# Kernel optimization log

Measured on AMD Instinct MI355X. Metric: run time of the kernel, lower is better.

Reference implementation:

```python
import jax, jax.numpy as jnp
import numpy as np

N_GRID = 64          # 64x64 grid of patches
N = N_GRID * N_GRID  # 4096 instances
L = 512
L2 = 1024
D = 128
NT = 10              # n_templates
EMB = 48 * 6 * 6     # 1728


def _conv(x, w, b):
    # x: (N,C,H,W), w: (O,I,kh,kw), VALID, stride 1
    y = jax.lax.conv_general_dilated(x, w, (1, 1), 'VALID',
                                     dimension_numbers=('NCHW', 'OIHW', 'NCHW'))
    return y + b[None, :, None, None]


def _maxpool2(x):
    return jax.lax.reduce_window(x, -jnp.inf, jax.lax.max,
                                 (1, 1, 2, 2), (1, 1, 2, 2), 'VALID')


def setup_inputs() -> dict:
    key = jax.random.key(0)
    ks = jax.random.split(key, 16)
    s = 0.05
    rr, cc = jnp.meshgrid(jnp.arange(N_GRID), jnp.arange(N_GRID), indexing='ij')
    positions = jnp.stack([rr.ravel(), cc.ravel()], axis=1).astype(jnp.int32)  # (N,2)
    return {
        'x': jax.random.normal(ks[0], (1, N, 3, 32, 32), jnp.float32),
        'positions': positions,
        'conv1_w': jax.random.normal(ks[1], (36, 3, 4, 4), jnp.float32) * s,
        'conv1_b': jnp.zeros((36,), jnp.float32),
        'conv2_w': jax.random.normal(ks[2], (48, 36, 3, 3), jnp.float32) * s,
        'conv2_b': jnp.zeros((48,), jnp.float32),
        'fc1_w': jax.random.normal(ks[3], (L, EMB), jnp.float32) * s,
        'fc1_b': jnp.zeros((L,), jnp.float32),
        'fc2_w': jax.random.normal(ks[4], (L, L), jnp.float32) * s,
        'fc2_b': jnp.zeros((L,), jnp.float32),
        'nbr_w': jax.random.normal(ks[5], (L, L), jnp.float32) * s,
        'nbr_b': jnp.zeros((L,), jnp.float32),
        'templates': jax.random.normal(ks[6], (NT, L2), jnp.float32),
        'proto_w': jax.random.normal(ks[7], (L2, L2), jnp.float32) * s,
        'proto_b': jnp.zeros((L2,), jnp.float32),
        'ga1_w': jax.random.normal(ks[8], (D, L2), jnp.float32) * s,
        'ga1_b': jnp.zeros((D,), jnp.float32),
        'ga2_w': jax.random.normal(ks[9], (1, D), jnp.float32) * s,
        'ga2_b': jnp.zeros((1,), jnp.float32),
        'cls_w': jax.random.normal(ks[10], (1, L2), jnp.float32) * s,
        'cls_b': jnp.zeros((1,), jnp.float32),
    }


def reference(x, positions, conv1_w, conv1_b, conv2_w, conv2_b,
              fc1_w, fc1_b, fc2_w, fc2_b, nbr_w, nbr_b, templates,
              proto_w, proto_b, ga1_w, ga1_b, ga2_w, ga2_b, cls_w, cls_b):
    temperature = 1.0
    xb = x[0]  # squeeze(0): (N,3,32,32)
    # feature_extractor_part1
    h = _maxpool2(jax.nn.relu(_conv(xb, conv1_w, conv1_b)))   # (N,36,14,14)
    h = _maxpool2(jax.nn.relu(_conv(h, conv2_w, conv2_b)))    # (N,48,6,6)
    h = h.reshape(-1, EMB)
    # feature_extractor_part2 (dropout = identity in eval)
    H = jax.nn.relu(h @ fc1_w.T + fc1_b)
    H = jax.nn.relu(H @ fc2_w.T + fc2_b)                       # (N,L)
    # neighbourhood attention (vectorized padded/masked form of the per-instance loop)
    p = positions.astype(jnp.int32)
    d0 = jnp.abs(p[:, 0][:, None] - p[:, 0][None, :])
    d1 = jnp.abs(p[:, 1][:, None] - p[:, 1][None, :])
    cheb = jnp.maximum(d0, d1)
    mask = (cheb > 0) & (cheb <= 1)                            # (N,N) bool, 8-neighborhood
    has_nbr = mask.any(axis=1)
    n = mask.shape[0]
    mask = jnp.where(has_nbr[:, None], mask, jnp.eye(n, dtype=bool))  # self fallback
    T = jnp.tanh(H @ nbr_w.T + nbr_b)                          # (N,L)
    S = H @ T.T                                                # S[i,j] = h_i . tanh(W h_j + b)
    logits = jnp.where(mask, S, jnp.finfo(S.dtype).min)
    alphas = jax.nn.softmax(logits, axis=1)                    # (N,N)
    nbhd = alphas @ H                                          # (N,L)
    H2 = jnp.concatenate([H, nbhd], axis=1)                    # (N,L2)
    # prototype attention
    P = jnp.tanh(H2 @ proto_w.T + proto_b)                     # (N,L2)
    betas = jax.nn.softmax((P @ templates.T).T / temperature, axis=1)  # (NT,N)
    embs = betas @ H2                                          # (NT,L2)
    # global attention
    g = jnp.tanh(embs @ ga1_w.T + ga1_b) @ ga2_w.T + ga2_b     # (NT,1)
    gammas = jax.nn.softmax(g.T / temperature, axis=1)         # (1,NT)
    M = gammas @ embs                                          # (1,L2)
    A = gammas @ betas                                         # (1,N)
    Y_prob = jax.nn.sigmoid(M @ cls_w.T + cls_b)               # (1,1)
    Y_hat = (Y_prob >= 0.5).astype(jnp.float32)
    return (Y_prob, Y_hat, A)
```

## Files before the change

### kernel.cpp

```cpp
#include <hip/hip_runtime.h>
#include <math.h>

#define NINST 4096

typedef _Float16 half8 __attribute__((ext_vector_type(8)));
typedef _Float16 half4 __attribute__((ext_vector_type(4)));
typedef float floatx4 __attribute__((ext_vector_type(4)));

__global__ void xform_w12(const float* __restrict__ w1, const float* __restrict__ w2,
                          _Float16* __restrict__ w1t, _Float16* __restrict__ w2t) {
  for (int i = blockIdx.x * 256 + threadIdx.x; i < 48 * 64; i += gridDim.x * 256) {
    const int oc = i >> 6, k = i & 63;
    const int ky = k >> 4, r = k & 15, kx = r >> 2, ic = r & 3;
    float v = 0.f;
    if (oc < 36 && ic < 3) v = w1[((oc * 3 + ic) * 4 + ky) * 4 + kx];
    w1t[i] = (_Float16)v;
  }
  for (int i = blockIdx.x * 256 + threadIdx.x; i < 3 * 48 * 128; i += gridDim.x * 256) {
    const int ky = i / 6144, r = i % 6144;
    const int oc = r >> 7, k = r & 127;
    float v = 0.f;
    if (k < 120) {
      const int kx = k / 40, ic = k % 40;
      if (ic < 36) v = w2[((oc * 36 + ic) * 3 + ky) * 3 + kx];
    }
    w2t[i] = (_Float16)v;
  }
}

__launch_bounds__(256, 4)
__global__ void conv_fused(const float* __restrict__ x,
                           const _Float16* __restrict__ w1t_g,
                           const _Float16* __restrict__ w2t_g,
                           const float* __restrict__ b1, const float* __restrict__ b2,
                           _Float16* __restrict__ emb) {
  __shared__ __align__(16) _Float16 x_s[4096];
  __shared__ __align__(16) _Float16 h1_s[7856];
  __shared__ __align__(16) _Float16 h2_s[1728];

  const int n = blockIdx.x, tid = threadIdx.x;
  const int lane = tid & 63, wave = tid >> 6;
  const int quad = lane >> 4, l15 = lane & 15;

  {
    const float* xb = x + (size_t)n * 3072 + tid * 4;
    floatx4 xr0 = __builtin_nontemporal_load((const floatx4*)(xb));
    floatx4 xr1 = __builtin_nontemporal_load((const floatx4*)(xb + 1024));
    floatx4 xr2 = __builtin_nontemporal_load((const floatx4*)(xb + 2048));
    half8 pk0, pk1;
    pk0[0] = (_Float16)xr0[0]; pk0[1] = (_Float16)xr1[0]; pk0[2] = (_Float16)xr2[0]; pk0[3] = (_Float16)0.f;
    pk0[4] = (_Float16)xr0[1]; pk0[5] = (_Float16)xr1[1]; pk0[6] = (_Float16)xr2[1]; pk0[7] = (_Float16)0.f;
    pk1[0] = (_Float16)xr0[2]; pk1[1] = (_Float16)xr1[2]; pk1[2] = (_Float16)xr2[2]; pk1[3] = (_Float16)0.f;
    pk1[4] = (_Float16)xr0[3]; pk1[5] = (_Float16)xr1[3]; pk1[6] = (_Float16)xr2[3]; pk1[7] = (_Float16)0.f;
    *(half8*)&x_s[tid * 16] = pk0;
    *(half8*)&x_s[tid * 16 + 8] = pk1;
    if (tid < 16) h1_s[7840 + tid] = (_Float16)0.f;
  }
  __syncthreads();

  {
    half8 bc[2][3];
#pragma unroll
    for (int c = 0; c < 2; c++)
#pragma unroll
      for (int nt = 0; nt < 3; nt++)
        bc[c][nt] = *(const half8*)&w1t_g[(nt * 16 + l15) * 64 + c * 32 + quad * 8];
    float bia[3];
#pragma unroll
    for (int nt = 0; nt < 3; nt++) {
      const int oc = nt * 16 + l15;
      bia[nt] = (oc < 36) ? b1[oc] : 0.f;
    }
    for (int mt = wave; mt < 49; mt += 4) {
      const int mA = mt * 16 + l15;
      const int ppA = mA >> 2, dA = mA & 3;
      const int yA = 2 * (ppA / 14) + (dA >> 1);
      const int xA = 2 * (ppA % 14) + (dA & 1);
      floatx4 a1[3];
#pragma unroll
      for (int nt = 0; nt < 3; nt++)
#pragma unroll
        for (int r = 0; r < 4; r++) a1[nt][r] = 0.f;
#pragma unroll
      for (int c = 0; c < 2; c++) {
        const int row = yA + c * 2 + (quad >> 1);
        const half8 af = *(const half8*)&x_s[row * 128 + xA * 4 + (quad & 1) * 8];
#pragma unroll
        for (int nt = 0; nt < 3; nt++)
          a1[nt] = __builtin_amdgcn_mfma_f32_16x16x32_f16(af, bc[c][nt], a1[nt], 0, 0, 0);
      }
      const int ppC = mt * 4 + quad;
#pragma unroll
      for (int nt = 0; nt < 3; nt++) {
        const int oc = nt * 16 + l15;
        float v = fmaxf(fmaxf(a1[nt][0], a1[nt][1]), fmaxf(a1[nt][2], a1[nt][3])) + bia[nt];
        v = fmaxf(v, 0.f);
        if (oc < 40) h1_s[ppC * 40 + oc] = (_Float16)v;
      }
    }
  }
  __syncthreads();

  floatx4 acc2[3][3];
#pragma unroll
  for (int a = 0; a < 3; a++)
#pragma unroll
    for (int j = 0; j < 3; j++)
#pragma unroll
      for (int r = 0; r < 4; r++) acc2[a][j][r] = 0.f;

  for (int ky = 0; ky < 3; ky++) {
    half8 bc2[4][3];
#pragma unroll
    for (int c = 0; c < 4; c++)
#pragma unroll
      for (int nt = 0; nt < 3; nt++)
        bc2[c][nt] = *(const half8*)&w2t_g[ky * 6144 + (nt * 16 + l15) * 128 + c * 32 + quad * 8];
#pragma unroll
    for (int mi = 0; mi < 3; mi++) {
      const int mt = wave + 4 * mi;
      if (mt < 9) {
        const int mA = mt * 16 + l15;
        const int ppA = mA >> 2, dA = mA & 3;
        const int y2 = 2 * (ppA / 6) + (dA >> 1);
        const int x2 = 2 * (ppA % 6) + (dA & 1);
        const int rb = ((y2 + ky) * 14 + x2) * 40;
#pragma unroll
        for (int c = 0; c < 4; c++) {
          const half8 af = *(const half8*)&h1_s[rb + c * 32 + quad * 8];
#pragma unroll
          for (int nt = 0; nt < 3; nt++)
            acc2[mi][nt] = __builtin_amdgcn_mfma_f32_16x16x32_f16(af, bc2[c][nt], acc2[mi][nt], 0, 0, 0);
        }
      }
    }
  }

  {
    float bia2[3];
#pragma unroll
    for (int nt = 0; nt < 3; nt++) bia2[nt] = b2[nt * 16 + l15];
#pragma unroll
    for (int mi = 0; mi < 3; mi++) {
      const int mt = wave + 4 * mi;
      if (mt < 9) {
        const int ppC = mt * 4 + quad;
#pragma unroll
        for (int nt = 0; nt < 3; nt++) {
          const int oc = nt * 16 + l15;
          float v = fmaxf(fmaxf(acc2[mi][nt][0], acc2[mi][nt][1]),
                          fmaxf(acc2[mi][nt][2], acc2[mi][nt][3])) + bia2[nt];
          v = fmaxf(v, 0.f);
          h2_s[oc * 36 + ppC] = (_Float16)v;
        }
      }
    }
  }
  __syncthreads();
  if (tid < 216) {
    half8* dst = (half8*)(emb + (size_t)n * 1728);
    dst[tid] = ((const half8*)h2_s)[tid];
  }
}

template <int ACT>
__launch_bounds__(256, 2)
__global__ void gemm_h(const _Float16* __restrict__ A, const float* __restrict__ Bf,
                       const float* __restrict__ bias, _Float16* __restrict__ C,
                       int K, int lda, int ldb, int ldc) {
  __shared__ __align__(16) _Float16 As[2][128 * 72];
  __shared__ __align__(16) _Float16 Bs[2][64 * 72];
  const int tid = threadIdx.x;
  const int m0 = blockIdx.y * 128, n0 = blockIdx.x * 64;
  const int lane = tid & 63, wave = tid >> 6;
  const int quad = lane >> 4, l15 = lane & 15;
  const int wm = (wave >> 1) * 64, wn = (wave & 1) * 32;
  const int arow = tid >> 1, acol = (tid & 1) * 32;
  const int brow = tid >> 2, bcol = (tid & 3) * 16;

  const _Float16* Ap = A + (size_t)(m0 + arow) * lda + acol;
  const float* Bp = Bf + (size_t)(n0 + brow) * ldb + bcol;

  half8 av0 = *(const half8*)(Ap);
  half8 av1 = *(const half8*)(Ap + 8);
  half8 av2 = *(const half8*)(Ap + 16);
  half8 av3 = *(const half8*)(Ap + 24);
  floatx4 bv0 = *(const floatx4*)(Bp);
  floatx4 bv1 = *(const floatx4*)(Bp + 4);
  floatx4 bv2 = *(const floatx4*)(Bp + 8);
  floatx4 bv3 = *(const floatx4*)(Bp + 12);

  floatx4 acc[4][2];
#pragma unroll
  for (int a = 0; a < 4; a++)
#pragma unroll
    for (int j = 0; j < 2; j++)
#pragma unroll
      for (int r = 0; r < 4; r++) acc[a][j][r] = 0.f;

  int buf = 0;
  for (int k0 = 0; k0 < K; k0 += 64) {
    *(half8*)&As[buf][arow * 72 + acol] = av0;
    *(half8*)&As[buf][arow * 72 + acol + 8] = av1;
    *(half8*)&As[buf][arow * 72 + acol + 16] = av2;
    *(half8*)&As[buf][arow * 72 + acol + 24] = av3;
    {
      half8 bh0, bh1;
      bh0[0] = (_Float16)bv0[0]; bh0[1] = (_Float16)bv0[1];
      bh0[2] = (_Float16)bv0[2]; bh0[3] = (_Float16)bv0[3];
      bh0[4] = (_Float16)bv1[0]; bh0[5] = (_Float16)bv1[1];
      bh0[6] = (_Float16)bv1[2]; bh0[7] = (_Float16)bv1[3];
      bh1[0] = (_Float16)bv2[0]; bh1[1] = (_Float16)bv2[1];
      bh1[2] = (_Float16)bv2[2]; bh1[3] = (_Float16)bv2[3];
      bh1[4] = (_Float16)bv3[0]; bh1[5] = (_Float16)bv3[1];
      bh1[6] = (_Float16)bv3[2]; bh1[7] = (_Float16)bv3[3];
      *(half8*)&Bs[buf][brow * 72 + bcol] = bh0;
      *(half8*)&Bs[buf][brow * 72 + bcol + 8] = bh1;
    }
    __syncthreads();
    if (k0 + 64 < K) {
      av0 = *(const half8*)(Ap + k0 + 64);
      av1 = *(const half8*)(Ap + k0 + 64 + 8);
      av2 = *(const half8*)(Ap + k0 + 64 + 16);
      av3 = *(const half8*)(Ap + k0 + 64 + 24);
      bv0 = *(const floatx4*)(Bp + k0 + 64);
      bv1 = *(const floatx4*)(Bp + k0 + 64 + 4);
      bv2 = *(const floatx4*)(Bp + k0 + 64 + 8);
      bv3 = *(const floatx4*)(Bp + k0 + 64 + 12);
    }
#pragma unroll
    for (int ks = 0; ks < 64; ks += 32) {
      half8 af[4], bf[2];
#pragma unroll
      for (int mt = 0; mt < 4; mt++)
        af[mt] = *(const half8*)&As[buf][(wm + mt * 16 + l15) * 72 + ks + quad * 8];
#pragma unroll
      for (int nt = 0; nt < 2; nt++)
        bf[nt] = *(const half8*)&Bs[buf][(wn + nt * 16 + l15) * 72 + ks + quad * 8];
#pragma unroll
      for (int mt = 0; mt < 4; mt++)
#pragma unroll
        for (int nt = 0; nt < 2; nt++)
          acc[mt][nt] = __builtin_amdgcn_mfma_f32_16x16x32_f16(af[mt], bf[nt], acc[mt][nt], 0, 0, 0);
    }
    buf ^= 1;
  }

#pragma unroll
  for (int nt = 0; nt < 2; nt++) {
    const int col = n0 + wn + nt * 16 + l15;
    const float bcolv = bias[col];
#pragma unroll
    for (int mt = 0; mt < 4; mt++) {
#pragma unroll
      for (int r = 0; r < 4; r++) {
        const int row = m0 + wm + mt * 16 + quad * 4 + r;
        float v = acc[mt][nt][r] + bcolv;
        if (ACT == 1) v = fmaxf(v, 0.f);
        if (ACT == 2) v = tanhf(v);
        C[(size_t)row * ldc + col] = (_Float16)v;
      }
    }
  }
}

__launch_bounds__(256)
__global__ void nbhd_k(_Float16* __restrict__ H2, const _Float16* __restrict__ T) {
  const int wid = (blockIdx.x * 256 + threadIdx.x) >> 6;
  const int lane = threadIdx.x & 63;
  const int r = wid >> 6, c = wid & 63;
  const _Float16* hi = H2 + (size_t)wid * 1024;
  float hreg[8];
#pragma unroll
  for (int u = 0; u < 8; u++) hreg[u] = (float)hi[u * 64 + lane];

  float sv[8];
  int jv[8];
  bool ok[8];
  int q = 0;
#pragma unroll
  for (int dr = -1; dr <= 1; dr++)
#pragma unroll
    for (int dc = -1; dc <= 1; dc++) {
      if (dr == 0 && dc == 0) continue;
      const int rr = r + dr, cc = c + dc;
      const bool v = (rr >= 0) && (rr < 64) && (cc >= 0) && (cc < 64);
      const int j = v ? (rr * 64 + cc) : wid;
      const _Float16* tj = T + (size_t)j * 512;
      float s = 0.f;
#pragma unroll
      for (int u = 0; u < 8; u++) s = fmaf(hreg[u], (float)tj[u * 64 + lane], s);
#pragma unroll
      for (int off = 32; off > 0; off >>= 1) s += __shfl_xor(s, off, 64);
      sv[q] = v ? s : -3.4e38f;
      jv[q] = j;
      ok[q] = v;
      q++;
    }

  float m = sv[0];
#pragma unroll
  for (int a = 1; a < 8; a++) m = fmaxf(m, sv[a]);
  float e[8], den = 0.f;
#pragma unroll
  for (int a = 0; a < 8; a++) {
    e[a] = ok[a] ? expf(sv[a] - m) : 0.f;
    den += e[a];
  }
  const float inv = 1.f / den;

  float outv[8];
#pragma unroll
  for (int u = 0; u < 8; u++) outv[u] = 0.f;
#pragma unroll
  for (int a = 0; a < 8; a++) {
    const float al = e[a] * inv;
    const _Float16* hj = H2 + (size_t)jv[a] * 1024;
#pragma unroll
    for (int u = 0; u < 8; u++) outv[u] = fmaf(al, (float)hj[u * 64 + lane], outv[u]);
  }
  _Float16* dst = H2 + (size_t)wid * 1024 + 512;
#pragma unroll
  for (int u = 0; u < 8; u++) dst[u * 64 + lane] = (_Float16)outv[u];
}

__launch_bounds__(256)
__global__ void templ_scores(const _Float16* __restrict__ P, const float* __restrict__ tmpl,
                             float* __restrict__ tl) {
  const int wid = (blockIdx.x * 256 + threadIdx.x) >> 6;
  const int lane = threadIdx.x & 63;
  const _Float16* p = P + (size_t)wid * 1024;
  float pr[16];
#pragma unroll
  for (int u = 0; u < 16; u++) pr[u] = (float)p[u * 64 + lane];
  for (int t = 0; t < 10; t++) {
    const float* tp = tmpl + t * 1024;
    float s = 0.f;
#pragma unroll
    for (int u = 0; u < 16; u++) s = fmaf(pr[u], tp[u * 64 + lane], s);
#pragma unroll
    for (int off = 32; off > 0; off >>= 1) s += __shfl_xor(s, off, 64);
    if (lane == 0) tl[t * NINST + wid] = s;
  }
}

__launch_bounds__(256)
__global__ void softmax_rows(const float* __restrict__ tl, float* __restrict__ betas,
                             float* __restrict__ embs) {
  const int t = blockIdx.x, tid = threadIdx.x;
  __shared__ float red[256];
  for (int i = tid; i < 1024; i += 256) embs[t * 1024 + i] = 0.f;
  const float* row = tl + t * NINST;
  float m = -3.4e38f;
  for (int i = tid; i < NINST; i += 256) m = fmaxf(m, row[i]);
  red[tid] = m;
  __syncthreads();
  for (int s = 128; s > 0; s >>= 1) {
    if (tid < s) red[tid] = fmaxf(red[tid], red[tid + s]);
    __syncthreads();
  }
  m = red[0];
  __syncthreads();
  float sum = 0.f;
  for (int i = tid; i < NINST; i += 256) sum += expf(row[i] - m);
  red[tid] = sum;
  __syncthreads();
  for (int s = 128; s > 0; s >>= 1) {
    if (tid < s) red[tid] += red[tid + s];
    __syncthreads();
  }
  const float inv = 1.f / red[0];
  for (int i = tid; i < NINST; i += 256) betas[t * NINST + i] = expf(row[i] - m) * inv;
}

__launch_bounds__(256)
__global__ void embs_k(const float* __restrict__ betas, const _Float16* __restrict__ H2,
                       float* __restrict__ embs) {
  const int k = blockIdx.x * 256 + threadIdx.x;
  const int nbase = blockIdx.y * 256;
  float acc[10];
#pragma unroll
  for (int t = 0; t < 10; t++) acc[t] = 0.f;
  for (int n = nbase; n < nbase + 256; n++) {
    const float v = (float)H2[(size_t)n * 1024 + k];
#pragma unroll
    for (int t = 0; t < 10; t++) acc[t] = fmaf(betas[t * NINST + n], v, acc[t]);
  }
#pragma unroll
  for (int t = 0; t < 10; t++) atomicAdd(&embs[t * 1024 + k], acc[t]);
}

__launch_bounds__(256)
__global__ void ga1_k(const float* __restrict__ embs, const float* __restrict__ ga1_w,
                      const float* __restrict__ ga1_b, float* __restrict__ hh) {
  const int d = blockIdx.x, tid = threadIdx.x;
  const int wave = tid >> 6, lane = tid & 63;
  __shared__ float part[4][10];

  float acc[10];
#pragma unroll
  for (int t = 0; t < 10; t++) acc[t] = 0.f;
#pragma unroll
  for (int kk = 0; kk < 4; kk++) {
    const int k = kk * 256 + tid;
    const float wv = ga1_w[(size_t)d * 1024 + k];
#pragma unroll
    for (int t = 0; t < 10; t++) acc[t] = fmaf(wv, embs[t * 1024 + k], acc[t]);
  }
#pragma unroll
  for (int t = 0; t < 10; t++) {
#pragma unroll
    for (int off = 32; off > 0; off >>= 1) acc[t] += __shfl_xor(acc[t], off, 64);
  }
  if (lane == 0) {
#pragma unroll
    for (int t = 0; t < 10; t++) part[wave][t] = acc[t];
  }
  __syncthreads();
  if (tid < 10) {
    const float s = part[0][tid] + part[1][tid] + part[2][tid] + part[3][tid];
    hh[tid * 128 + d] = tanhf(s + ga1_b[d]);
  }
}

__launch_bounds__(256)
__global__ void ga2_k(const float* __restrict__ hh, const float* __restrict__ ga2_w,
                      const float* __restrict__ ga2_b, const float* __restrict__ embs,
                      const float* __restrict__ cls_w, const float* __restrict__ cls_b,
                      float* __restrict__ gam_ws, float* __restrict__ out) {
  __shared__ float g_s[10], gam_s[10];
  __shared__ float red[256];
  const int tid = threadIdx.x;
  const int wave = tid >> 6, lane = tid & 63;

  if (wave == 0) {
    for (int t = 0; t < 10; t++) {
      float s = hh[t * 128 + lane] * ga2_w[lane] + hh[t * 128 + 64 + lane] * ga2_w[64 + lane];
#pragma unroll
      for (int off = 32; off > 0; off >>= 1) s += __shfl_xor(s, off, 64);
      if (lane == 0) g_s[t] = s + ga2_b[0];
    }
  }
  __syncthreads();
  if (tid == 0) {
    float m = g_s[0];
    for (int t = 1; t < 10; t++) m = fmaxf(m, g_s[t]);
    float sum = 0.f;
    for (int t = 0; t < 10; t++) sum += expf(g_s[t] - m);
    for (int t = 0; t < 10; t++) {
      gam_s[t] = expf(g_s[t] - m) / sum;
      gam_ws[t] = gam_s[t];
    }
  }
  __syncthreads();

  float partl = 0.f;
  for (int k = tid; k < 1024; k += 256) {
    float a = 0.f;
#pragma unroll
    for (int t = 0; t < 10; t++) a = fmaf(gam_s[t], embs[t * 1024 + k], a);
    partl = fmaf(a, cls_w[k], partl);
  }
  red[tid] = partl;
  __syncthreads();
  for (int s = 128; s > 0; s >>= 1) {
    if (tid < s) red[tid] += red[tid + s];
    __syncthreads();
  }
  if (tid == 0) {
    const float z = red[0] + cls_b[0];
    const float yp = 1.f / (1.f + expf(-z));
    out[0] = yp;
    out[1] = (yp >= 0.5f) ? 1.f : 0.f;
  }
}

__launch_bounds__(256)
__global__ void a_k(const float* __restrict__ betas, const float* __restrict__ gam,
                    float* __restrict__ outA) {
  const int n = blockIdx.x * 256 + threadIdx.x;
  float a = 0.f;
#pragma unroll
  for (int t = 0; t < 10; t++) a = fmaf(gam[t], betas[t * NINST + n], a);
  outA[n] = a;
}

extern "C" void kernel_launch(void* const* d_in, const int* in_sizes, int n_in,
                              void* d_out, int out_size, void* d_ws, size_t ws_size,
                              hipStream_t stream) {
  const float* x       = (const float*)d_in[0];
  const float* w1      = (const float*)d_in[2];
  const float* b1      = (const float*)d_in[3];
  const float* w2      = (const float*)d_in[4];
  const float* b2      = (const float*)d_in[5];
  const float* fc1_w   = (const float*)d_in[6];
  const float* fc1_b   = (const float*)d_in[7];
  const float* fc2_w   = (const float*)d_in[8];
  const float* fc2_b   = (const float*)d_in[9];
  const float* nbr_w   = (const float*)d_in[10];
  const float* nbr_b   = (const float*)d_in[11];
  const float* tmpl    = (const float*)d_in[12];
  const float* proto_w = (const float*)d_in[13];
  const float* proto_b = (const float*)d_in[14];
  const float* ga1_w   = (const float*)d_in[15];
  const float* ga1_b   = (const float*)d_in[16];
  const float* ga2_w   = (const float*)d_in[17];
  const float* ga2_b   = (const float*)d_in[18];
  const float* cls_w   = (const float*)d_in[19];
  const float* cls_b   = (const float*)d_in[20];
  float* out = (float*)d_out;

  char* w = (char*)d_ws;
  _Float16* embh = (_Float16*)w;  w += (size_t)4096 * 1728 * 2;
  _Float16* H1h  = (_Float16*)w;  w += (size_t)4096 * 512 * 2;
  _Float16* H2h  = (_Float16*)w;  w += (size_t)4096 * 1024 * 2;
  _Float16* TbH  = (_Float16*)w;  w += (size_t)4096 * 512 * 2;
  _Float16* PH   = (_Float16*)w;  w += (size_t)4096 * 1024 * 2;
  _Float16* w1tG = (_Float16*)w;  w += (size_t)48 * 64 * 2;
  _Float16* w2tG = (_Float16*)w;  w += (size_t)3 * 48 * 128 * 2;
  float* tl   = (float*)w;        w += (size_t)10 * NINST * 4;
  float* bet  = (float*)w;        w += (size_t)10 * NINST * 4;
  float* embs = (float*)w;        w += (size_t)10 * 1024 * 4;
  float* hhw  = (float*)w;        w += (size_t)10 * 128 * 4;
  float* gam  = (float*)w;        w += 256;

  xform_w12<<<64, 256, 0, stream>>>(w1, w2, w1tG, w2tG);
  conv_fused<<<NINST, 256, 0, stream>>>(x, w1tG, w2tG, b1, b2, embh);

  gemm_h<1><<<dim3(8, 32), 256, 0, stream>>>(embh, fc1_w, fc1_b, H1h, 1728, 1728, 1728, 512);
  gemm_h<1><<<dim3(8, 32), 256, 0, stream>>>(H1h, fc2_w, fc2_b, H2h, 512, 512, 512, 1024);
  gemm_h<2><<<dim3(8, 32), 256, 0, stream>>>(H2h, nbr_w, nbr_b, TbH, 512, 1024, 512, 512);
  nbhd_k<<<1024, 256, 0, stream>>>(H2h, TbH);
  gemm_h<2><<<dim3(16, 32), 256, 0, stream>>>(H2h, proto_w, proto_b, PH, 1024, 1024, 1024, 1024);
  templ_scores<<<1024, 256, 0, stream>>>(PH, tmpl, tl);
  softmax_rows<<<10, 256, 0, stream>>>(tl, bet, embs);
  embs_k<<<dim3(4, 16), 256, 0, stream>>>(bet, H2h, embs);
  ga1_k<<<128, 256, 0, stream>>>(embs, ga1_w, ga1_b, hhw);
  ga2_k<<<1, 256, 0, stream>>>(hhw, ga2_w, ga2_b, embs, cls_w, cls_b, gam, out);
  a_k<<<16, 256, 0, stream>>>(bet, gam, out + 2);
}
```

Baseline: 369.1 us.

## Fuse template scoring into proto GEMM, shrink GEMM tiles, batch conv instances

After: 381.5 us. +3.4%, slower.

```diff
diff --git a/kernel.cpp b/kernel.cpp
--- a/kernel.cpp
+++ b/kernel.cpp
@@ -8,7 +8,8 @@
 typedef float floatx4 __attribute__((ext_vector_type(4)));
 
 __global__ void xform_w12(const float* __restrict__ w1, const float* __restrict__ w2,
-                          _Float16* __restrict__ w1t, _Float16* __restrict__ w2t) {
+                          _Float16* __restrict__ w1t, _Float16* __restrict__ w2t,
+                          float* __restrict__ tl) {
   for (int i = blockIdx.x * 256 + threadIdx.x; i < 48 * 64; i += gridDim.x * 256) {
     const int oc = i >> 6, k = i & 63;
     const int ky = k >> 4, r = k & 15, kx = r >> 2, ic = r & 3;
@@ -26,35 +27,39 @@
     }
     w2t[i] = (_Float16)v;
   }
-}
-
-__launch_bounds__(256, 4)
+  for (int i = blockIdx.x * 256 + threadIdx.x; i < 10 * NINST; i += gridDim.x * 256)
+    tl[i] = 0.f;
+}
+
+__launch_bounds__(256, 2)
 __global__ void conv_fused(const float* __restrict__ x,
                            const _Float16* __restrict__ w1t_g,
                            const _Float16* __restrict__ w2t_g,
                            const float* __restrict__ b1, const float* __restrict__ b2,
                            _Float16* __restrict__ emb) {
-  __shared__ __align__(16) _Float16 x_s[4096];
-  __shared__ __align__(16) _Float16 h1_s[7856];
-  __shared__ __align__(16) _Float16 h2_s[1728];
-
-  const int n = blockIdx.x, tid = threadIdx.x;
+  __shared__ __align__(16) _Float16 x_s[8192];
+  __shared__ __align__(16) _Float16 h1_s[15712];
+
+  const int n0 = blockIdx.x * 2, tid = threadIdx.x;
   const int lane = tid & 63, wave = tid >> 6;
   const int quad = lane >> 4, l15 = lane & 15;
 
   {
-    const float* xb = x + (size_t)n * 3072 + tid * 4;
-    floatx4 xr0 = __builtin_nontemporal_load((const floatx4*)(xb));
-    floatx4 xr1 = __builtin_nontemporal_load((const floatx4*)(xb + 1024));
-    floatx4 xr2 = __builtin_nontemporal_load((const floatx4*)(xb + 2048));
-    half8 pk0, pk1;
-    pk0[0] = (_Float16)xr0[0]; pk0[1] = (_Float16)xr1[0]; pk0[2] = (_Float16)xr2[0]; pk0[3] = (_Float16)0.f;
-    pk0[4] = (_Float16)xr0[1]; pk0[5] = (_Float16)xr1[1]; pk0[6] = (_Float16)xr2[1]; pk0[7] = (_Float16)0.f;
-    pk1[0] = (_Float16)xr0[2]; pk1[1] = (_Float16)xr1[2]; pk1[2] = (_Float16)xr2[2]; pk1[3] = (_Float16)0.f;
-    pk1[4] = (_Float16)xr0[3]; pk1[5] = (_Float16)xr1[3]; pk1[6] = (_Float16)xr2[3]; pk1[7] = (_Float16)0.f;
-    *(half8*)&x_s[tid * 16] = pk0;
-    *(half8*)&x_s[tid * 16 + 8] = pk1;
-    if (tid < 16) h1_s[7840 + tid] = (_Float16)0.f;
+#pragma unroll
+    for (int inst = 0; inst < 2; inst++) {
+      const float* xb = x + (size_t)(n0 + inst) * 3072 + tid * 4;
+      floatx4 xr0 = __builtin_nontemporal_load((const floatx4*)(xb));
+      floatx4 xr1 = __builtin_nontemporal_load((const floatx4*)(xb + 1024));
+      floatx4 xr2 = __builtin_nontemporal_load((const floatx4*)(xb + 2048));
+      half8 pk0, pk1;
+      pk0[0] = (_Float16)xr0[0]; pk0[1] = (_Float16)xr1[0]; pk0[2] = (_Float16)xr2[0]; pk0[3] = (_Float16)0.f;
+      pk0[4] = (_Float16)xr0[1]; pk0[5] = (_Float16)xr1[1]; pk0[6] = (_Float16)xr2[1]; pk0[7] = (_Float16)0.f;
+      pk1[0] = (_Float16)xr0[2]; pk1[1] = (_Float16)xr1[2]; pk1[2] = (_Float16)xr2[2]; pk1[3] = (_Float16)0.f;
+      pk1[4] = (_Float16)xr0[3]; pk1[5] = (_Float16)xr1[3]; pk1[6] = (_Float16)xr2[3]; pk1[7] = (_Float16)0.f;
+      *(half8*)&x_s[inst * 4096 + tid * 16] = pk0;
+      *(half8*)&x_s[inst * 4096 + tid * 16 + 8] = pk1;
+    }
+    if (tid < 16) { h1_s[7840 + tid] = (_Float16)0.f; h1_s[7856 + 7840 + tid] = (_Float16)0.f; }
   }
   __syncthreads();
 
@@ -71,75 +76,83 @@
       const int oc = nt * 16 + l15;
       bia[nt] = (oc < 36) ? b1[oc] : 0.f;
     }
-    for (int mt = wave; mt < 49; mt += 4) {
-      const int mA = mt * 16 + l15;
-      const int ppA = mA >> 2, dA = mA & 3;
-      const int yA = 2 * (ppA / 14) + (dA >> 1);
-      const int xA = 2 * (ppA % 14) + (dA & 1);
-      floatx4 a1[3];
-#pragma unroll
-      for (int nt = 0; nt < 3; nt++)
-#pragma unroll
-        for (int r = 0; r < 4; r++) a1[nt][r] = 0.f;
-#pragma unroll
-      for (int c = 0; c < 2; c++) {
-        const int row = yA + c * 2 + (quad >> 1);
-        const half8 af = *(const half8*)&x_s[row * 128 + xA * 4 + (quad & 1) * 8];
-#pragma unroll
-        for (int nt = 0; nt < 3; nt++)
-          a1[nt] = __builtin_amdgcn_mfma_f32_16x16x32_f16(af, bc[c][nt], a1[nt], 0, 0, 0);
-      }
-      const int ppC = mt * 4 + quad;
-#pragma unroll
-      for (int nt = 0; nt < 3; nt++) {
-        const int oc = nt * 16 + l15;
-        float v = fmaxf(fmaxf(a1[nt][0], a1[nt][1]), fmaxf(a1[nt][2], a1[nt][3])) + bia[nt];
-        v = fmaxf(v, 0.f);
-        if (oc < 40) h1_s[ppC * 40 + oc] = (_Float16)v;
-      }
-    }
-  }
-  __syncthreads();
-
-  floatx4 acc2[3][3];
-#pragma unroll
-  for (int a = 0; a < 3; a++)
-#pragma unroll
-    for (int j = 0; j < 3; j++)
-#pragma unroll
-      for (int r = 0; r < 4; r++) acc2[a][j][r] = 0.f;
-
-  for (int ky = 0; ky < 3; ky++) {
-    half8 bc2[4][3];
-#pragma unroll
-    for (int c = 0; c < 4; c++)
-#pragma unroll
-      for (int nt = 0; nt < 3; nt++)
-        bc2[c][nt] = *(const half8*)&w2t_g[ky * 6144 + (nt * 16 + l15) * 128 + c * 32 + quad * 8];
-#pragma unroll
-    for (int mi = 0; mi < 3; mi++) {
-      const int mt = wave + 4 * mi;
-      if (mt < 9) {
+#pragma unroll
+    for (int inst = 0; inst < 2; inst++) {
+      const _Float16* xin = x_s + inst * 4096;
+      _Float16* h1o = h1_s + inst * 7856;
+      for (int mt = wave; mt < 49; mt += 4) {
         const int mA = mt * 16 + l15;
         const int ppA = mA >> 2, dA = mA & 3;
-        const int y2 = 2 * (ppA / 6) + (dA >> 1);
-        const int x2 = 2 * (ppA % 6) + (dA & 1);
-        const int rb = ((y2 + ky) * 14 + x2) * 40;
-#pragma unroll
-        for (int c = 0; c < 4; c++) {
-          const half8 af = *(const half8*)&h1_s[rb + c * 32 + quad * 8];
+        const int yA = 2 * (ppA / 14) + (dA >> 1);
+        const int xA = 2 * (ppA % 14) + (dA & 1);
+        floatx4 a1[3];
+#pragma unroll
+        for (int nt = 0; nt < 3; nt++)
+#pragma unroll
+          for (int r = 0; r < 4; r++) a1[nt][r] = 0.f;
+#pragma unroll
+        for (int c = 0; c < 2; c++) {
+          const int row = yA + c * 2 + (quad >> 1);
+          const half8 af = *(const half8*)&xin[row * 128 + xA * 4 + (quad & 1) * 8];
 #pragma unroll
           for (int nt = 0; nt < 3; nt++)
-            acc2[mi][nt] = __builtin_amdgcn_mfma_f32_16x16x32_f16(af, bc2[c][nt], acc2[mi][nt], 0, 0, 0);
+            a1[nt] = __builtin_amdgcn_mfma_f32_16x16x32_f16(af, bc[c][nt], a1[nt], 0, 0, 0);
+        }
+        const int ppC = mt * 4 + quad;
+#pragma unroll
+        for (int nt = 0; nt < 3; nt++) {
+          const int oc = nt * 16 + l15;
+          float v = fmaxf(fmaxf(a1[nt][0], a1[nt][1]), fmaxf(a1[nt][2], a1[nt][3])) + bia[nt];
+          v = fmaxf(v, 0.f);
+          if (oc < 40) h1o[ppC * 40 + oc] = (_Float16)v;
         }
       }
     }
   }
-
-  {
-    float bia2[3];
-#pragma unroll
-    for (int nt = 0; nt < 3; nt++) bia2[nt] = b2[nt * 16 + l15];
+  __syncthreads();
+
+  float bia2[3];
+#pragma unroll
+  for (int nt = 0; nt < 3; nt++) bia2[nt] = b2[nt * 16 + l15];
+
+#pragma unroll
+  for (int inst = 0; inst < 2; inst++) {
+    const _Float16* h1i = h1_s + inst * 7856;
+    _Float16* h2o = x_s + inst * 1728;
+    floatx4 acc2[3][3];
+#pragma unroll
+    for (int a = 0; a < 3; a++)
+#pragma unroll
+      for (int j = 0; j < 3; j++)
+#pragma unroll
+        for (int r = 0; r < 4; r++) acc2[a][j][r] = 0.f;
+
+    for (int ky = 0; ky < 3; ky++) {
+      half8 bc2[4][3];
+#pragma unroll
+      for (int c = 0; c < 4; c++)
+#pragma unroll
+        for (int nt = 0; nt < 3; nt++)
+          bc2[c][nt] = *(const half8*)&w2t_g[ky * 6144 + (nt * 16 + l15) * 128 + c * 32 + quad * 8];
+#pragma unroll
+      for (int mi = 0; mi < 3; mi++) {
+        const int mt = wave + 4 * mi;
+        if (mt < 9) {
+          const int mA = mt * 16 + l15;
+          const int ppA = mA >> 2, dA = mA & 3;
+          const int y2 = 2 * (ppA / 6) + (dA >> 1);
+          const int x2 = 2 * (ppA % 6) + (dA & 1);
+          const int rb = ((y2 + ky) * 14 + x2) * 40;
+#pragma unroll
+          for (int c = 0; c < 4; c++) {
+            const half8 af = *(const half8*)&h1i[rb + c * 32 + quad * 8];
+#pragma unroll
+            for (int nt = 0; nt < 3; nt++)
+              acc2[mi][nt] = __builtin_amdgcn_mfma_f32_16x16x32_f16(af, bc2[c][nt], acc2[mi][nt], 0, 0, 0);
+          }
+        }
+      }
+    }
 #pragma unroll
     for (int mi = 0; mi < 3; mi++) {
       const int mt = wave + 4 * mi;
@@ -151,48 +164,53 @@
           float v = fmaxf(fmaxf(acc2[mi][nt][0], acc2[mi][nt][1]),
                           fmaxf(acc2[mi][nt][2], acc2[mi][nt][3])) + bia2[nt];
           v = fmaxf(v, 0.f);
-          h2_s[oc * 36 + ppC] = (_Float16)v;
+          h2o[oc * 36 + ppC] = (_Float16)v;
         }
       }
     }
   }
   __syncthreads();
-  if (tid < 216) {
-    half8* dst = (half8*)(emb + (size_t)n * 1728);
-    dst[tid] = ((const half8*)h2_s)[tid];
-  }
-}
-
-template <int ACT>
+  {
+    half8* dst = (half8*)(emb + (size_t)n0 * 1728);
+    const half8* src = (const half8*)x_s;
+    for (int i = tid; i < 432; i += 256) dst[i] = src[i];
+  }
+}
+
+template <int ACT, bool FUSE>
 __launch_bounds__(256, 2)
 __global__ void gemm_h(const _Float16* __restrict__ A, const float* __restrict__ Bf,
                        const float* __restrict__ bias, _Float16* __restrict__ C,
-                       int K, int lda, int ldb, int ldc) {
-  __shared__ __align__(16) _Float16 As[2][128 * 72];
+                       int K, int lda, int ldb, int ldc,
+                       const float* __restrict__ tmpl, float* __restrict__ tl) {
+  __shared__ __align__(16) _Float16 As[2][64 * 72];
   __shared__ __align__(16) _Float16 Bs[2][64 * 72];
+  __shared__ float tmpl_s[640];
   const int tid = threadIdx.x;
-  const int m0 = blockIdx.y * 128, n0 = blockIdx.x * 64;
+  const int m0 = blockIdx.y * 64, n0 = blockIdx.x * 64;
   const int lane = tid & 63, wave = tid >> 6;
   const int quad = lane >> 4, l15 = lane & 15;
-  const int wm = (wave >> 1) * 64, wn = (wave & 1) * 32;
-  const int arow = tid >> 1, acol = (tid & 1) * 32;
-  const int brow = tid >> 2, bcol = (tid & 3) * 16;
-
-  const _Float16* Ap = A + (size_t)(m0 + arow) * lda + acol;
-  const float* Bp = Bf + (size_t)(n0 + brow) * ldb + bcol;
+  const int wm = (wave >> 1) * 32, wn = (wave & 1) * 32;
+  const int srow = tid >> 2, scol = (tid & 3) * 16;
+
+  if (FUSE) {
+    for (int i = tid; i < 640; i += 256)
+      tmpl_s[i] = tmpl[(i >> 6) * 1024 + n0 + (i & 63)];
+  }
+
+  const _Float16* Ap = A + (size_t)(m0 + srow) * lda + scol;
+  const float* Bp = Bf + (size_t)(n0 + srow) * ldb + scol;
 
   half8 av0 = *(const half8*)(Ap);
   half8 av1 = *(const half8*)(Ap + 8);
-  half8 av2 = *(const half8*)(Ap + 16);
-  half8 av3 = *(const half8*)(Ap + 24);
   floatx4 bv0 = *(const floatx4*)(Bp);
   floatx4 bv1 = *(const floatx4*)(Bp + 4);
   floatx4 bv2 = *(const floatx4*)(Bp + 8);
   floatx4 bv3 = *(const floatx4*)(Bp + 12);
 
-  floatx4 acc[4][2];
-#pragma unroll
-  for (int a = 0; a < 4; a++)
+  floatx4 acc[2][2];
+#pragma unroll
+  for (int a = 0; a < 2; a++)
 #pragma unroll
     for (int j = 0; j < 2; j++)
 #pragma unroll
@@ -200,10 +218,8 @@
 
   int buf = 0;
   for (int k0 = 0; k0 < K; k0 += 64) {
-    *(half8*)&As[buf][arow * 72 + acol] = av0;
-    *(half8*)&As[buf][arow * 72 + acol + 8] = av1;
-    *(half8*)&As[buf][arow * 72 + acol + 16] = av2;
-    *(half8*)&As[buf][arow * 72 + acol + 24] = av3;
+    *(half8*)&As[buf][srow * 72 + scol] = av0;
+    *(half8*)&As[buf][srow * 72 + scol + 8] = av1;
     {
       half8 bh0, bh1;
       bh0[0] = (_Float16)bv0[0]; bh0[1] = (_Float16)bv0[1];
@@ -214,15 +230,13 @@
       bh1[2] = (_Float16)bv2[2]; bh1[3] = (_Float16)bv2[3];
       bh1[4] = (_Float16)bv3[0]; bh1[5] = (_Float16)bv3[1];
       bh1[6] = (_Float16)bv3[2]; bh1[7] = (_Float16)bv3[3];
-      *(half8*)&Bs[buf][brow * 72 + bcol] = bh0;
-      *(half8*)&Bs[buf][brow * 72 + bcol + 8] = bh1;
+      *(half8*)&Bs[buf][srow * 72 + scol] = bh0;
+      *(half8*)&Bs[buf][srow * 72 + scol + 8] = bh1;
     }
     __syncthreads();
     if (k0 + 64 < K) {
       av0 = *(const half8*)(Ap + k0 + 64);
       av1 = *(const half8*)(Ap + k0 + 64 + 8);
-      av2 = *(const half8*)(Ap + k0 + 64 + 16);
-      av3 = *(const half8*)(Ap + k0 + 64 + 24);
       bv0 = *(const floatx4*)(Bp + k0 + 64);
       bv1 = *(const floatx4*)(Bp + k0 + 64 + 4);
       bv2 = *(const floatx4*)(Bp + k0 + 64 + 8);
@@ -230,15 +244,15 @@
     }
 #pragma unroll
     for (int ks = 0; ks < 64; ks += 32) {
-      half8 af[4], bf[2];
-#pragma unroll
-      for (int mt = 0; mt < 4; mt++)
+      half8 af[2], bf[2];
+#pragma unroll
+      for (int mt = 0; mt < 2; mt++)
         af[mt] = *(const half8*)&As[buf][(wm + mt * 16 + l15) * 72 + ks + quad * 8];
 #pragma unroll
       for (int nt = 0; nt < 2; nt++)
         bf[nt] = *(const half8*)&Bs[buf][(wn + nt * 16 + l15) * 72 + ks + quad * 8];
 #pragma unroll
-      for (int mt = 0; mt < 4; mt++)
+      for (int mt = 0; mt < 2; mt++)
 #pragma unroll
         for (int nt = 0; nt < 2; nt++)
           acc[mt][nt] = __builtin_amdgcn_mfma_f32_16x16x32_f16(af[mt], bf[nt], acc[mt][nt], 0, 0, 0);
@@ -248,18 +262,45 @@
 
 #pragma unroll
   for (int nt = 0; nt < 2; nt++) {
-    const int col = n0 + wn + nt * 16 + l15;
-    const float bcolv = bias[col];
-#pragma unroll
-    for (int mt = 0; mt < 4; mt++) {
+    const float bcolv = bias[n0 + wn + nt * 16 + l15];
+#pragma unroll
+    for (int mt = 0; mt < 2; mt++)
 #pragma unroll
       for (int r = 0; r < 4; r++) {
-        const int row = m0 + wm + mt * 16 + quad * 4 + r;
         float v = acc[mt][nt][r] + bcolv;
         if (ACT == 1) v = fmaxf(v, 0.f);
         if (ACT == 2) v = tanhf(v);
-        C[(size_t)row * ldc + col] = (_Float16)v;
+        acc[mt][nt][r] = v;
       }
+  }
+
+  if (!FUSE) {
+#pragma unroll
+    for (int nt = 0; nt < 2; nt++) {
+      const int col = n0 + wn + nt * 16 + l15;
+#pragma unroll
+      for (int mt = 0; mt < 2; mt++)
+#pragma unroll
+        for (int r = 0; r < 4; r++)
+          C[(size_t)(m0 + wm + mt * 16 + quad * 4 + r) * ldc + col] = (_Float16)acc[mt][nt][r];
+    }
+  } else {
+#pragma unroll
+    for (int t = 0; t < 10; t++) {
+      const float t0 = tmpl_s[t * 64 + wn + l15];
+      const float t1 = tmpl_s[t * 64 + wn + 16 + l15];
+#pragma unroll
+      for (int mt = 0; mt < 2; mt++)
+#pragma unroll
+        for (int r = 0; r < 4; r++) {
+          float p = acc[mt][0][r] * t0 + acc[mt][1][r] * t1;
+          p += __shfl_xor(p, 1, 64);
+          p += __shfl_xor(p, 2, 64);
+          p += __shfl_xor(p, 4, 64);
+          p += __shfl_xor(p, 8, 64);
+          if (l15 == 0)
+            atomicAdd(&tl[t * NINST + m0 + wm + mt * 16 + quad * 4 + r], p);
+        }
     }
   }
 }
@@ -269,10 +310,7 @@
   const int wid = (blockIdx.x * 256 + threadIdx.x) >> 6;
   const int lane = threadIdx.x & 63;
   const int r = wid >> 6, c = wid & 63;
-  const _Float16* hi = H2 + (size_t)wid * 1024;
-  float hreg[8];
-#pragma unroll
-  for (int u = 0; u < 8; u++) hreg[u] = (float)hi[u * 64 + lane];
+  const half8 hv = *(const half8*)&H2[(size_t)wid * 1024 + lane * 8];
 
   float sv[8];
   int jv[8];
@@ -286,10 +324,10 @@
       const int rr = r + dr, cc = c + dc;
       const bool v = (rr >= 0) && (rr < 64) && (cc >= 0) && (cc < 64);
       const int j = v ? (rr * 64 + cc) : wid;
-      const _Float16* tj = T + (size_t)j * 512;
+      const half8 tv = *(const half8*)&T[(size_t)j * 512 + lane * 8];
       float s = 0.f;
 #pragma unroll
-      for (int u = 0; u < 8; u++) s = fmaf(hreg[u], (float)tj[u * 64 + lane], s);
+      for (int u = 0; u < 8; u++) s = fmaf((float)hv[u], (float)tv[u], s);
 #pragma unroll
       for (int off = 32; off > 0; off >>= 1) s += __shfl_xor(s, off, 64);
       sv[q] = v ? s : -3.4e38f;
@@ -309,39 +347,20 @@
   }
   const float inv = 1.f / den;
 
-  float outv[8];
-#pragma unroll
-  for (int u = 0; u < 8; u++) outv[u] = 0.f;
+  float ov[8];
+#pragma unroll
+  for (int u = 0; u < 8; u++) ov[u] = 0.f;
 #pragma unroll
   for (int a = 0; a < 8; a++) {
     const float al = e[a] * inv;
-    const _Float16* hj = H2 + (size_t)jv[a] * 1024;
-#pragma unroll
-    for (int u = 0; u < 8; u++) outv[u] = fmaf(al, (float)hj[u * 64 + lane], outv[u]);
-  }
-  _Float16* dst = H2 + (size_t)wid * 1024 + 512;
-#pragma unroll
-  for (int u = 0; u < 8; u++) dst[u * 64 + lane] = (_Float16)outv[u];
-}
-
-__launch_bounds__(256)
-__global__ void templ_scores(const _Float16* __restrict__ P, const float* __restrict__ tmpl,
-                             float* __restrict__ tl) {
-  const int wid = (blockIdx.x * 256 + threadIdx.x) >> 6;
-  const int lane = threadIdx.x & 63;
-  const _Float16* p = P + (size_t)wid * 1024;
-  float pr[16];
-#pragma unroll
-  for (int u = 0; u < 16; u++) pr[u] = (float)p[u * 64 + lane];
-  for (int t = 0; t < 10; t++) {
-    const float* tp = tmpl + t * 1024;
-    float s = 0.f;
-#pragma unroll
-    for (int u = 0; u < 16; u++) s = fmaf(pr[u], tp[u * 64 + lane], s);
-#pragma unroll
-    for (int off = 32; off > 0; off >>= 1) s += __shfl_xor(s, off, 64);
-    if (lane == 0) tl[t * NINST + wid] = s;
-  }
+    const half8 hj = *(const half8*)&H2[(size_t)jv[a] * 1024 + lane * 8];
+#pragma unroll
+    for (int u = 0; u < 8; u++) ov[u] = fmaf(al, (float)hj[u], ov[u]);
+  }
+  half8 pk;
+#pragma unroll
+  for (int u = 0; u < 8; u++) pk[u] = (_Float16)ov[u];
+  *(half8*)&H2[(size_t)wid * 1024 + 512 + lane * 8] = pk;
 }
 
 __launch_bounds__(256)
@@ -515,7 +534,6 @@
   _Float16* H1h  = (_Float16*)w;  w += (size_t)4096 * 512 * 2;
   _Float16* H2h  = (_Float16*)w;  w += (size_t)4096 * 1024 * 2;
   _Float16* TbH  = (_Float16*)w;  w += (size_t)4096 * 512 * 2;
-  _Float16* PH   = (_Float16*)w;  w += (size_t)4096 * 1024 * 2;
   _Float16* w1tG = (_Float16*)w;  w += (size_t)48 * 64 * 2;
   _Float16* w2tG = (_Float16*)w;  w += (size_t)3 * 48 * 128 * 2;
   float* tl   = (float*)w;        w += (size_t)10 * NINST * 4;
@@ -524,15 +542,18 @@
   float* hhw  = (float*)w;        w += (size_t)10 * 128 * 4;
   float* gam  = (float*)w;        w += 256;
 
-  xform_w12<<<64, 256, 0, stream>>>(w1, w2, w1tG, w2tG);
-  conv_fused<<<NINST, 256, 0, stream>>>(x, w1tG, w2tG, b1, b2, embh);
-
-  gemm_h<1><<<dim3(8, 32), 256, 0, stream>>>(embh, fc1_w, fc1_b, H1h, 1728, 1728, 1728, 512);
-  gemm_h<1><<<dim3(8, 32), 256, 0, stream>>>(H1h, fc2_w, fc2_b, H2h, 512, 512, 512, 1024);
-  gemm_h<2><<<dim3(8, 32), 256, 0, stream>>>(H2h, nbr_w, nbr_b, TbH, 512, 1024, 512, 512);
+  xform_w12<<<64, 256, 0, stream>>>(w1, w2, w1tG, w2tG, tl);
+  conv_fused<<<NINST / 2, 256, 0, stream>>>(x, w1tG, w2tG, b1, b2, embh);
+
+  gemm_h<1, false><<<dim3(8, 64), 256, 0, stream>>>(embh, fc1_w, fc1_b, H1h,
+                                                    1728, 1728, 1728, 512, nullptr, nullptr);
+  gemm_h<1, false><<<dim3(8, 64), 256, 0, stream>>>(H1h, fc2_w, fc2_b, H2h,
+                                                    512, 512, 512, 1024, nullptr, nullptr);
+  gemm_h<2, false><<<dim3(8, 64), 256, 0, stream>>>(H2h, nbr_w, nbr_b, TbH,
+                                                    512, 1024, 512, 512, nullptr, nullptr);
   nbhd_k<<<1024, 256, 0, stream>>>(H2h, TbH);
-  gemm_h<2><<<dim3(16, 32), 256, 0, stream>>>(H2h, proto_w, proto_b, PH, 1024, 1024, 1024, 1024);
-  templ_scores<<<1024, 256, 0, stream>>>(PH, tmpl, tl);
+  gemm_h<2, true><<<dim3(16, 64), 256, 0, stream>>>(H2h, proto_w, proto_b, nullptr,
+                                                    1024, 1024, 1024, 0, tmpl, tl);
   softmax_rows<<<10, 256, 0, stream>>>(tl, bet, embs);
   embs_k<<<dim3(4, 16), 256, 0, stream>>>(bet, H2h, embs);
   ga1_k<<<128, 256, 0, stream>>>(embs, ga1_w, ga1_b, hhw);
```
